# Kernel tuning notes

Measured on AMD Instinct MI355X. Metric: run time of the kernel, lower is better.

The kernel has to match this reference:

```python
import jax, jax.numpy as jnp
import numpy as np

C = 64; H = 80; W = 120; B = 2; V = 3; BV = B * V; D = 20
NEAR = 0.1; FAR = 100.0
BF16 = jnp.bfloat16


def conv2d(x, w, b, pad):
    y = jax.lax.conv_general_dilated(x, w, (1, 1), [(pad, pad), (pad, pad)],
                                     dimension_numbers=('NCHW', 'OIHW', 'NCHW'))
    return y + b[None, :, None, None]


def bn2d(x, g, b, m, v, eps=1e-5):
    # BatchNorm2d in inference mode (running stats)
    scale = g / jnp.sqrt(v + eps)
    return (x - m[None, :, None, None]) * scale[None, :, None, None] + b[None, :, None, None]


def grid_sample(feat, grid):
    # feat [N,C,Hf,Wf], grid [N,Hg,Wg,2] in [-1,1]; bilinear, zeros padding, align_corners=True
    _, _, Hf, Wf = feat.shape
    gx = (grid[..., 0] + 1.0) * 0.5 * (Wf - 1)
    gy = (grid[..., 1] + 1.0) * 0.5 * (Hf - 1)
    x0 = jnp.floor(gx); y0 = jnp.floor(gy)

    def one(f, gx, gy, x0, y0):
        def gather(xi, yi):
            valid = (xi >= 0) & (xi < Wf) & (yi >= 0) & (yi < Hf)
            xc = jnp.clip(xi, 0, Wf - 1).astype(jnp.int32)
            yc = jnp.clip(yi, 0, Hf - 1).astype(jnp.int32)
            return f[:, yc, xc] * valid.astype(f.dtype)
        wx = gx - x0; wy = gy - y0
        return (gather(x0, y0) * ((1 - wx) * (1 - wy))
                + gather(x0 + 1, y0) * (wx * (1 - wy))
                + gather(x0, y0 + 1) * ((1 - wx) * wy)
                + gather(x0 + 1, y0 + 1) * (wx * wy))
    return jax.vmap(one)(feat, gx, gy, x0, y0)


def forward(x, intrinsics, c2ws,
            pf_bn1_g, pf_bn1_b, pf_bn1_m, pf_bn1_v, pf_w1, pf_b1,
            pf_bn2_g, pf_bn2_b, pf_bn2_m, pf_bn2_v, pf_w2, pf_b2,
            cp_w, cp_b, cf_bn_g, cf_bn_b, cf_bn_m, cf_bn_v, cf_w, cf_b):
    # ---- flag[0]: predicted depth -> world xyz, position_fusion ----
    depth = 255.0 * (0.5 * jnp.tanh(x[:, 0]) + 0.5)                       # [BV,H,W]
    d16 = depth.astype(BF16)
    ug = jnp.broadcast_to(jnp.arange(W, dtype=jnp.float32)[None, :], (H, W)).astype(BF16)
    vg = jnp.broadcast_to(jnp.arange(H, dtype=jnp.float32)[:, None], (H, W)).astype(BF16)
    cam = jnp.stack([ug[None] * d16, vg[None] * d16, d16], axis=-1).reshape(BV, H * W, 3)
    Kinv = jnp.linalg.inv(intrinsics.astype(jnp.float32)).astype(BF16)
    xyz = jnp.einsum('nij,npj->npi', Kinv, cam)                           # cam coords
    xyz = jnp.einsum('nij,npj->npi', c2ws[:, :3, :3].astype(BF16), xyz) \
          + c2ws[:, :3, 3].astype(BF16)[:, None, :]                       # world coords
    xyz = xyz.reshape(BV, H, W, 3).transpose(0, 3, 1, 2).astype(x.dtype)
    h = jnp.concatenate([xyz, x], axis=1)                                 # [BV,C+3,H,W]
    h = jax.nn.silu(conv2d(bn2d(h, pf_bn1_g, pf_bn1_b, pf_bn1_m, pf_bn1_v), pf_w1, pf_b1, 4))
    h = jax.nn.silu(conv2d(bn2d(h, pf_bn2_g, pf_bn2_b, pf_bn2_m, pf_bn2_v), pf_w2, pf_b2, 4))

    # ---- flag[1]: multi-view plane-sweep correlation ----
    xr = h.reshape(B, V, C, H, W)
    vb = lambda t: t.transpose(1, 0, 2, 3, 4).reshape(BV, C, H, W)        # 'b v ... -> (v b) ...'
    feat01 = vb(xr)
    Ki = intrinsics.reshape(B, V, 3, 3)
    intr_curr = jax.lax.stop_gradient(
        (Ki * jnp.array([W, H, 1.0], jnp.float32)[None, None, :, None]).transpose(1, 0, 2, 3).reshape(BV, 3, 3))
    E = jax.lax.stop_gradient(c2ws.reshape(B, V, 4, 4))
    Einv = jnp.linalg.inv(E)
    dmin, dmax = 1.0 / FAR, 1.0 / NEAR
    depth_vals = 1.0 / (dmin + jnp.linspace(0.0, 1.0, D) * (dmax - dmin))  # [D]
    pix = jnp.stack([jnp.broadcast_to(jnp.arange(W, dtype=jnp.float32)[None, :], (H, W)),
                     jnp.broadcast_to(jnp.arange(H, dtype=jnp.float32)[:, None], (H, W)),
                     jnp.ones((H, W), jnp.float32)], 0).reshape(3, H * W)
    Kinv_c = jnp.linalg.inv(intr_curr).astype(BF16)

    corr = 0.0
    for idx in range(1, V):
        order = list(range(V))[idx:] + list(range(V))[:idx]
        feat10 = vb(xr[:, jnp.array(order)])                              # [BV,C,H,W]
        pose = jnp.concatenate([E[:, o] @ Einv[:, v0] for v0, o in enumerate(order)], axis=0)  # [BV,4,4]
        pts = jnp.einsum('bij,jp->bip', Kinv_c, pix.astype(BF16))
        pts = jnp.einsum('bij,bjp->bip', pose[:, :3, :3].astype(BF16), pts)
        pts = pts[:, :, None, :] * depth_vals.astype(BF16)[None, None, :, None] \
              + pose[:, :3, 3].astype(BF16)[:, :, None, None]             # [BV,3,D,HW]
        pts = jnp.einsum('bij,bjdp->bidp', intr_curr.astype(BF16), pts).astype(jnp.float32)
        den = jnp.maximum(pts[:, 2], 1e-3)
        grid = jnp.stack([2.0 * pts[:, 0] / den / (W - 1) - 1.0,
                          2.0 * pts[:, 1] / den / (H - 1) - 1.0], axis=-1)
        grid = jax.lax.stop_gradient(grid.reshape(BV, D * H, W, 2))
        warped = grid_sample(feat10, grid).reshape(BV, C, D, H, W)
        corr = corr + jnp.einsum('bchw,bcdhw->bdhw', feat01, warped) / (C ** 0.5)
    corr = corr / (V - 1)

    cin = jnp.concatenate([corr, feat01], axis=1)                         # [BV,D+C,H,W]
    cost = conv2d(cin, cp_w, cp_b, 1).reshape(V, B, C, H, W).transpose(1, 0, 2, 3, 4)
    fused = jnp.concatenate([cost, xr], axis=2).reshape(BV, 2 * C, H, W)
    out = jax.nn.silu(conv2d(bn2d(fused, cf_bn_g, cf_bn_b, cf_bn_m, cf_bn_v), cf_w, cf_b, 4))
    return out


def setup_inputs() -> dict:
    key = jax.random.key(0)
    ks = jax.random.split(key, 24)
    def nrm(i, shape, scale=1.0):
        return scale * jax.random.normal(ks[i], shape, jnp.float32)
    def wconv(i, shape):
        fan_in = int(np.prod(shape[1:]))
        return jax.random.normal(ks[i], shape, jnp.float32) / np.sqrt(fan_in)
    x = nrm(0, (BV, C, H, W))
    Kmat = np.tile(np.array([[1.2, 0, 0.5], [0, 1.6, 0.5], [0, 0, 1.0]], np.float32), (BV, 1, 1))
    intrinsics = jnp.asarray(Kmat)
    c2_list = []
    for i in range(BV):
        th = 0.3 * (i % V) - 0.3
        T = np.eye(4, dtype=np.float32)
        T[:3, :3] = np.array([[np.cos(th), 0, np.sin(th)], [0, 1, 0], [-np.sin(th), 0, np.cos(th)]], np.float32)
        T[:3, 3] = [0.5 * (i % V) - 0.5, 0.0, 0.1]
        c2_list.append(T)
    c2ws = jnp.asarray(np.stack(c2_list))
    # first BN sees raw world-xyz channels (magnitude ~1e4), so realistic running var there
    bn1_v = jnp.concatenate([jnp.full((3,), 1e8, jnp.float32), jnp.ones((C,), jnp.float32)])
    return dict(
        x=x, intrinsics=intrinsics, c2ws=c2ws,
        pf_bn1_g=1.0 + 0.1 * nrm(1, (C + 3,)), pf_bn1_b=0.1 * nrm(2, (C + 3,)),
        pf_bn1_m=0.1 * nrm(3, (C + 3,)), pf_bn1_v=bn1_v,
        pf_w1=wconv(4, (C, C + 3, 9, 9)), pf_b1=0.01 * nrm(5, (C,)),
        pf_bn2_g=1.0 + 0.1 * nrm(6, (C,)), pf_bn2_b=0.1 * nrm(7, (C,)),
        pf_bn2_m=0.1 * nrm(8, (C,)), pf_bn2_v=jnp.ones((C,), jnp.float32),
        pf_w2=wconv(9, (C, C, 9, 9)), pf_b2=0.01 * nrm(10, (C,)),
        cp_w=wconv(11, (C, C + D, 3, 3)), cp_b=0.01 * nrm(12, (C,)),
        cf_bn_g=1.0 + 0.1 * nrm(13, (2 * C,)), cf_bn_b=0.1 * nrm(14, (2 * C,)),
        cf_bn_m=0.1 * nrm(15, (2 * C,)), cf_bn_v=jnp.ones((2 * C,), jnp.float32),
        cf_w=wconv(16, (C, 2 * C, 9, 9)), cf_b=0.01 * nrm(17, (C,)))


def reference(x, intrinsics, c2ws,
              pf_bn1_g, pf_bn1_b, pf_bn1_m, pf_bn1_v, pf_w1, pf_b1,
              pf_bn2_g, pf_bn2_b, pf_bn2_m, pf_bn2_v, pf_w2, pf_b2,
              cp_w, cp_b, cf_bn_g, cf_bn_b, cf_bn_m, cf_bn_v, cf_w, cf_b):
    return forward(x, intrinsics, c2ws,
                   pf_bn1_g, pf_bn1_b, pf_bn1_m, pf_bn1_v, pf_w1, pf_b1,
                   pf_bn2_g, pf_bn2_b, pf_bn2_m, pf_bn2_v, pf_w2, pf_b2,
                   cp_w, cp_b, cf_bn_g, cf_bn_b, cf_bn_m, cf_bn_v, cf_w, cf_b)
```

## Files before the change

kernel.cpp:

```cpp
#include <hip/hip_runtime.h>
#include <math.h>

static constexpr int kH  = 80;
static constexpr int kW  = 120;
static constexpr int kHW = kH * kW;
static constexpr int kBV = 6;
static constexpr int kD  = 20;

typedef __attribute__((ext_vector_type(8)))  short bf16x8;
typedef __attribute__((ext_vector_type(16))) float f32x16;
typedef __attribute__((ext_vector_type(4)))  int   i32x4;
typedef __attribute__((ext_vector_type(2)))  int   i32x2;
typedef __attribute__((ext_vector_type(4)))  float float4v;

__device__ __forceinline__ float bf16r(float x) {
  unsigned u = __float_as_uint(x);
  u += 0x7FFFu + ((u >> 16) & 1u);
  return __uint_as_float(u & 0xFFFF0000u);
}
__device__ __forceinline__ unsigned short bf16c(float x) {
  unsigned u = __float_as_uint(x);
  u += 0x7FFFu + ((u >> 16) & 1u);
  return (unsigned short)(u >> 16);
}
__device__ __forceinline__ int pack2(float a, float b) {
  return (int)((unsigned)bf16c(a) | ((unsigned)bf16c(b) << 16));
}
__device__ __forceinline__ float bl(unsigned pk) {
  return __uint_as_float(pk << 16);
}
__device__ __forceinline__ float bh(unsigned pk) {
  return __uint_as_float(pk & 0xFFFF0000u);
}

struct ConstBuf {
  float bn1_s[67], bn1_o[67];
  float bn2_s[64], bn2_o[64];
  float bnf_s[128], bnf_o[128];
  float Kinv[6][9];
  float Rw[6][9];
  float tw[6][3];
  float Kinvc[6][9];
  float intrc[6][9];
  float poseR[2][6][9];
  float poseT[2][6][3];
  float dvals[20];
};

__device__ void inv3x3(const float* A, float* o) {
  float a = A[0], b = A[1], c = A[2];
  float d = A[3], e = A[4], f = A[5];
  float g = A[6], h = A[7], i = A[8];
  float det = a * (e * i - f * h) - b * (d * i - f * g) + c * (d * h - e * g);
  float id = 1.0f / det;
  o[0] = (e * i - f * h) * id;
  o[1] = -(b * i - c * h) * id;
  o[2] = (b * f - c * e) * id;
  o[3] = -(d * i - f * g) * id;
  o[4] = (a * i - c * g) * id;
  o[5] = -(a * f - c * d) * id;
  o[6] = (d * h - e * g) * id;
  o[7] = -(a * h - b * g) * id;
  o[8] = (a * e - b * d) * id;
}

__device__ void inv4x4(const float* A, float* out) {
  float M[4][8];
  for (int r = 0; r < 4; ++r) {
    for (int c = 0; c < 4; ++c) M[r][c] = A[r * 4 + c];
    for (int c = 0; c < 4; ++c) M[r][4 + c] = (r == c) ? 1.0f : 0.0f;
  }
  for (int col = 0; col < 4; ++col) {
    int p = col;
    float best = fabsf(M[col][col]);
    for (int r = col + 1; r < 4; ++r) {
      float v = fabsf(M[r][col]);
      if (v > best) { best = v; p = r; }
    }
    if (p != col)
      for (int c = 0; c < 8; ++c) { float t = M[col][c]; M[col][c] = M[p][c]; M[p][c] = t; }
    float inv = 1.0f / M[col][col];
    for (int c = 0; c < 8; ++c) M[col][c] *= inv;
    for (int r = 0; r < 4; ++r) {
      if (r == col) continue;
      float f = M[r][col];
      for (int c = 0; c < 8; ++c) M[r][c] -= f * M[col][c];
    }
  }
  for (int r = 0; r < 4; ++r)
    for (int c = 0; c < 4; ++c) out[r * 4 + c] = M[r][4 + c];
}

__device__ void mm4(const float* A, const float* B, float* C) {
  for (int r = 0; r < 4; ++r)
    for (int c = 0; c < 4; ++c) {
      float s = 0.0f;
      for (int k = 0; k < 4; ++k) s += A[r * 4 + k] * B[k * 4 + c];
      C[r * 4 + c] = s;
    }
}

__global__ void consts_kernel(const float* __restrict__ intr, const float* __restrict__ c2,
                              const float* g1, const float* b1, const float* m1, const float* v1,
                              const float* g2, const float* b2, const float* m2, const float* v2,
                              const float* gf, const float* bff, const float* mf, const float* vff,
                              ConstBuf* cb) {
  int tid = threadIdx.x;
  for (int c = tid; c < 67; c += 64) {
    float s = g1[c] / sqrtf(v1[c] + 1e-5f);
    cb->bn1_s[c] = s; cb->bn1_o[c] = b1[c] - m1[c] * s;
  }
  for (int c = tid; c < 64; c += 64) {
    float s = g2[c] / sqrtf(v2[c] + 1e-5f);
    cb->bn2_s[c] = s; cb->bn2_o[c] = b2[c] - m2[c] * s;
  }
  for (int c = tid; c < 128; c += 64) {
    float s = gf[c] / sqrtf(vff[c] + 1e-5f);
    cb->bnf_s[c] = s; cb->bnf_o[c] = bff[c] - mf[c] * s;
  }
  if (tid < 20) {
    float l = (1.0f / 19.0f) * (float)tid;
    cb->dvals[tid] = bf16r(1.0f / (0.01f + l * 9.99f));
  }
  __shared__ float Einv_s[6][16];
  if (tid < 6) {
    float Ki[9];
    inv3x3(intr + tid * 9, Ki);
    for (int k = 0; k < 9; ++k) cb->Kinv[tid][k] = bf16r(Ki[k]);
    const float* T = c2 + tid * 16;
    cb->Rw[tid][0] = bf16r(T[0]);  cb->Rw[tid][1] = bf16r(T[1]);  cb->Rw[tid][2] = bf16r(T[2]);
    cb->Rw[tid][3] = bf16r(T[4]);  cb->Rw[tid][4] = bf16r(T[5]);  cb->Rw[tid][5] = bf16r(T[6]);
    cb->Rw[tid][6] = bf16r(T[8]);  cb->Rw[tid][7] = bf16r(T[9]);  cb->Rw[tid][8] = bf16r(T[10]);
    cb->tw[tid][0] = bf16r(T[3]);  cb->tw[tid][1] = bf16r(T[7]);  cb->tw[tid][2] = bf16r(T[11]);
    inv4x4(T, Einv_s[tid]);
    int vj = tid >> 1, bj = tid & 1, ii = bj * 3 + vj;
    const float* Kk = intr + ii * 9;
    float S[9] = {Kk[0] * 120.0f, Kk[1] * 120.0f, Kk[2] * 120.0f,
                  Kk[3] * 80.0f,  Kk[4] * 80.0f,  Kk[5] * 80.0f,
                  Kk[6],          Kk[7],          Kk[8]};
    for (int k = 0; k < 9; ++k) cb->intrc[tid][k] = bf16r(S[k]);
    float Si[9];
    inv3x3(S, Si);
    for (int k = 0; k < 9; ++k) cb->Kinvc[tid][k] = bf16r(Si[k]);
  }
  __syncthreads();
  if (tid < 12) {
    int t = tid / 6, jj = tid % 6;
    int vj = jj >> 1, bj = jj & 1;
    int o = (vj + t + 1) % 3;
    float P[16];
    mm4(c2 + (bj * 3 + o) * 16, Einv_s[bj * 3 + vj], P);
    for (int r = 0; r < 3; ++r) {
      for (int c = 0; c < 3; ++c) cb->poseR[t][jj][r * 3 + c] = bf16r(P[r * 4 + c]);
      cb->poseT[t][jj][r] = bf16r(P[r * 4 + 3]);
    }
  }
}

template <int K, int CINP, int CINR>
__global__ __launch_bounds__(256)
void prep_w(const float* __restrict__ w, unsigned short* __restrict__ Wp) {
  constexpr int NCH = CINP / 32;
  constexpr int NU = K * K * NCH * 256;
  int u = blockIdx.x * 256 + threadIdx.x;
  if (u >= NU) return;
  int slot = u & 255;
  int rest = u >> 8;
  int ci = rest % NCH;
  int kk = rest / NCH;
  int ky = kk / K, kx = kk - ky * K;
  int oc = slot >> 2;
  int gi = (slot & 3) ^ ((oc >> 2) & 3);
  int chb = ci * 32 + gi * 8;
  unsigned short o[8];
#pragma unroll
  for (int e = 0; e < 8; ++e) {
    int ch = chb + e;
    float val = (ch < CINR) ? w[(((size_t)oc * CINR + ch) * K + ky) * K + kx] : 0.0f;
    o[e] = bf16c(val);
  }
  i32x4 pk;
  pk.x = (int)o[0] | ((int)o[1] << 16);
  pk.y = (int)o[2] | ((int)o[3] << 16);
  pk.z = (int)o[4] | ((int)o[5] << 16);
  pk.w = (int)o[6] | ((int)o[7] << 16);
  *(i32x4*)&Wp[(size_t)u * 8] = pk;
}

__global__ __launch_bounds__(256)
void hn_pack(const float* __restrict__ x, const ConstBuf* __restrict__ cb,
             unsigned short* __restrict__ hn_b) {
  int id = blockIdx.x * 256 + threadIdx.x;
  if (id >= kBV * kHW) return;
  int bv = id / kHW, pix = id - bv * kHW;
  int yy = pix / kW, xx = pix - yy * kW;
  float t0 = tanhf(x[(size_t)bv * 64 * kHW + pix]);
  float depth = 255.0f * (0.5f * t0 + 0.5f);
  float dz = bf16r(depth);
  float cx = bf16r((float)xx * dz);
  float cy = bf16r((float)yy * dz);
  const float* Ki = cb->Kinv[bv];
  float p0 = bf16r(Ki[0] * cx + Ki[1] * cy + Ki[2] * dz);
  float p1 = bf16r(Ki[3] * cx + Ki[4] * cy + Ki[5] * dz);
  float p2 = bf16r(Ki[6] * cx + Ki[7] * cy + Ki[8] * dz);
  const float* R = cb->Rw[bv];
  const float* tw = cb->tw[bv];
  float q[3];
  q[0] = bf16r(bf16r(R[0] * p0 + R[1] * p1 + R[2] * p2) + tw[0]);
  q[1] = bf16r(bf16r(R[3] * p0 + R[4] * p1 + R[5] * p2) + tw[1]);
  q[2] = bf16r(bf16r(R[6] * p0 + R[7] * p1 + R[8] * p2) + tw[2]);
  unsigned short* o = &hn_b[(size_t)id * 96];
  const float* xb = x + (size_t)bv * 64 * kHW + pix;
#pragma unroll
  for (int g = 0; g < 24; ++g) {
    float vv[4];
#pragma unroll
    for (int e = 0; e < 4; ++e) {
      int ch = g * 4 + e;
      float val;
      if (ch < 3) val = q[ch] * cb->bn1_s[ch] + cb->bn1_o[ch];
      else if (ch < 67) val = xb[(size_t)(ch - 3) * kHW] * cb->bn1_s[ch] + cb->bn1_o[ch];
      else val = 0.0f;
      vv[e] = val;
    }
    i32x2 pk = {pack2(vv[0], vv[1]), pack2(vv[2], vv[3])};
    *(i32x2*)(o + g * 4) = pk;
  }
}

template <int CINP, int K, int OUT>
__global__ __launch_bounds__(256)
void conv_mfma(const unsigned short* __restrict__ in_b,
               const unsigned short* __restrict__ Wp,
               const float* __restrict__ bias,
               const ConstBuf* __restrict__ cb,
               float* __restrict__ outf,
               unsigned short* __restrict__ outb,
               unsigned short* __restrict__ outb2) {
  constexpr int NCH = CINP / 32;
  constexpr int KK = K * K;
  constexpr int GN = KK / 3;
  constexpr int PAD = K / 2;
  constexpr int NC = 16 + K - 1;
  constexpr int NR = 8 + K - 1;
  constexpr int NPX = NC * NR;
  __shared__ unsigned short sA[NPX * 32];
  __shared__ unsigned short sB[2][3 * 2048];

  const int tid = threadIdx.x;
  const int w = tid >> 6, l = tid & 63;
  const int bx = blockIdx.x, by = blockIdx.y, bz = blockIdx.z;
  const size_t inbase = (size_t)bz * kHW;

  const int r = l & 31, h = l >> 5;
  const int xloc = r & 15;
  const int ybase = 2 * w + (r >> 4);
  f32x16 acc[2] = {};

  int boff[2][2];
#pragma unroll
  for (int nt = 0; nt < 2; ++nt)
#pragma unroll
    for (int kc = 0; kc < 2; ++kc) {
      int oc = nt * 32 + (l & 31);
      int gi = kc * 2 + h;
      boff[nt][kc] = (oc * 4 + (gi ^ ((oc >> 2) & 3))) * 8;
    }

  for (int ci = 0; ci < NCH; ++ci) {
    for (int g2 = tid; g2 < NPX * 4; g2 += 256) {
      int px = g2 >> 2, gi = g2 & 3;
      int hy = px / NC, hx = px - hy * NC;
      int gy = by * 8 - PAD + hy, gx = bx * 16 - PAD + hx;
      bool ok = ((unsigned)gy < (unsigned)kH) && ((unsigned)gx < (unsigned)kW);
      i32x4 v = {0, 0, 0, 0};
      if (ok) v = *(const i32x4*)&in_b[(inbase + gy * kW + gx) * CINP + ci * 32 + gi * 8];
      *(i32x4*)&sA[px * 32 + ((gi ^ ((px >> 2) & 3)) << 3)] = v;
    }
#pragma unroll
    for (int t = 0; t < 3; ++t) {
      int u = tid + t * 256;
      int kki = u >> 8, slot = u & 255;
      *(i32x4*)&sB[0][u * 8] =
          *(const i32x4*)&Wp[(((size_t)kki * NCH + ci) * 256 + slot) * 8];
    }
    __syncthreads();

    for (int g = 0; g < GN; ++g) {
      const int cur = g & 1, nxt = cur ^ 1;
      const bool hasnext = (g + 1 < GN);
      i32x4 pf[3];
      if (hasnext) {
#pragma unroll
        for (int t = 0; t < 3; ++t) {
          int u = tid + t * 256;
          int kki = u >> 8, slot = u & 255;
          pf[t] = *(const i32x4*)
              &Wp[(((size_t)((g + 1) * 3 + kki) * NCH + ci) * 256 + slot) * 8];
        }
      }
#pragma unroll
      for (int kki = 0; kki < 3; ++kki) {
        const int kk = g * 3 + kki;
        const int ky = kk / K, kx = kk - ky * K;
        const int hp = (ybase + ky) * NC + (xloc + kx);
        bf16x8 a[2];
#pragma unroll
        for (int kc = 0; kc < 2; ++kc) {
          int gi = kc * 2 + h;
          a[kc] = *(const bf16x8*)&sA[hp * 32 + ((gi ^ ((hp >> 2) & 3)) << 3)];
        }
        bf16x8 bb[2][2];
#pragma unroll
        for (int nt = 0; nt < 2; ++nt)
#pragma unroll
          for (int kc = 0; kc < 2; ++kc)
            bb[nt][kc] = *(const bf16x8*)&sB[cur][kki * 2048 + boff[nt][kc]];
#pragma unroll
        for (int nt = 0; nt < 2; ++nt) {
          acc[nt] = __builtin_amdgcn_mfma_f32_32x32x16_bf16(a[0], bb[nt][0], acc[nt], 0, 0, 0);
          acc[nt] = __builtin_amdgcn_mfma_f32_32x32x16_bf16(a[1], bb[nt][1], acc[nt], 0, 0, 0);
        }
      }
      if (hasnext) {
#pragma unroll
        for (int t = 0; t < 3; ++t)
          *(i32x4*)&sB[nxt][(tid + t * 256) * 8] = pf[t];
      }
      __syncthreads();
    }
  }

#pragma unroll
  for (int nt = 0; nt < 2; ++nt) {
    const int oc = nt * 32 + (l & 31);
    const float bs = bias[oc];
    float s2 = 0.f, o2 = 0.f;
    if (OUT == 0) { s2 = cb->bn2_s[oc]; o2 = cb->bn2_o[oc]; }
    if (OUT == 1) { s2 = cb->bnf_s[64 + oc]; o2 = cb->bnf_o[64 + oc]; }
    if (OUT == 2) { s2 = cb->bnf_s[oc]; o2 = cb->bnf_o[oc]; }
#pragma unroll
    for (int reg = 0; reg < 16; ++reg) {
      int row = (reg & 3) + 8 * (reg >> 2) + 4 * h;
      int x = bx * 16 + (row & 15);
      if (x >= kW) continue;
      int y = by * 8 + 2 * w + (row >> 4);
      float v = acc[nt][reg] + bs;
      if (OUT != 2) v = v / (1.0f + expf(-v));
      if (OUT == 0) {
        size_t px = inbase + y * kW + x;
        outb[px * 64 + oc] = bf16c(v * s2 + o2);
      } else if (OUT == 1) {
        size_t px = inbase + y * kW + x;
        outb[px * 64 + oc] = bf16c(v);
        outb2[px * 128 + 64 + oc] = bf16c(v * s2 + o2);
      } else if (OUT == 2) {
        int i = (bz & 1) * 3 + (bz >> 1);
        size_t px = (size_t)i * kHW + y * kW + x;
        outb[px * 128 + oc] = bf16c(v * s2 + o2);
      } else {
        outf[((size_t)bz * 64 + oc) * kHW + y * kW + x] = v;
      }
    }
  }
}

__global__ __launch_bounds__(256)
void corr_kernel(const unsigned short* __restrict__ h_b, const ConstBuf* __restrict__ cb,
                 unsigned short* __restrict__ cin_b) {
  __shared__ float sgeo[4][2][40][8];
  const int tid = threadIdx.x;
  const int w = tid >> 6, lane = tid & 63;
  const int pair = blockIdx.x * 4 + w;
  const int j = pair / (kHW / 2);
  const int pix = (pair - j * (kHW / 2)) * 2;
  const int b = j & 1, v = j >> 1;
  const int ph = lane >> 5, cl = lane & 31;
  const int pixl = pix + ph;
  const int dst = b * 3 + v;
  const unsigned f01pk =
      ((const unsigned*)(h_b + ((size_t)dst * kHW + pixl) * 64))[cl];
  const float f01lo = bl(f01pk), f01hi = bh(f01pk);
  const char* sb0 = (const char*)(h_b + (size_t)(b * 3 + ((v + 1) % 3)) * kHW * 64);
  const char* sb1 = (const char*)(h_b + (size_t)(b * 3 + ((v + 2) % 3)) * kHW * 64);

  for (int job = lane; job < 80; job += 64) {
    const int p = job / 40, jj = job - p * 40;
    const int d = jj >> 1, t = jj & 1;
    const int pp = pix + p;
    const int yyp = pp / kW, xxp = pp - yyp * kW;
    const float* Kc = cb->Kinvc[j];
    const float* IC = cb->intrc[j];
    const float uf = (float)xxp, vf = (float)yyp;
    float p1_0 = bf16r(Kc[0] * uf + Kc[1] * vf + Kc[2]);
    float p1_1 = bf16r(Kc[3] * uf + Kc[4] * vf + Kc[5]);
    float p1_2 = bf16r(Kc[6] * uf + Kc[7] * vf + Kc[8]);
    const float* PR = cb->poseR[t][j];
    const float* PT = cb->poseT[t][j];
    float p20 = bf16r(PR[0] * p1_0 + PR[1] * p1_1 + PR[2] * p1_2);
    float p21 = bf16r(PR[3] * p1_0 + PR[4] * p1_1 + PR[5] * p1_2);
    float p22 = bf16r(PR[6] * p1_0 + PR[7] * p1_1 + PR[8] * p1_2);
    float dv = cb->dvals[d];
    float q0 = bf16r(bf16r(p20 * dv) + PT[0]);
    float q1 = bf16r(bf16r(p21 * dv) + PT[1]);
    float q2 = bf16r(bf16r(p22 * dv) + PT[2]);
    float s0 = bf16r(IC[0] * q0 + IC[1] * q1 + IC[2] * q2);
    float s1 = bf16r(IC[3] * q0 + IC[4] * q1 + IC[5] * q2);
    float s2 = bf16r(IC[6] * q0 + IC[7] * q1 + IC[8] * q2);
    float den = fmaxf(s2, 1e-3f);
    float g0 = 2.0f * s0 / den / 119.0f - 1.0f;
    float g1 = 2.0f * s1 / den / 79.0f - 1.0f;
    float gx = (g0 + 1.0f) * 0.5f * 119.0f;
    float gy = (g1 + 1.0f) * 0.5f * 79.0f;
    float x0f = floorf(gx), y0f = floorf(gy);
    float wx = gx - x0f, wy = gy - y0f;
    float x1f = x0f + 1.0f, y1f = y0f + 1.0f;
    float vx0 = (x0f >= 0.0f && x0f < 120.0f) ? 1.0f : 0.0f;
    float vx1 = (x1f >= 0.0f && x1f < 120.0f) ? 1.0f : 0.0f;
    float vy0 = (y0f >= 0.0f && y0f < 80.0f) ? 1.0f : 0.0f;
    float vy1 = (y1f >= 0.0f && y1f < 80.0f) ? 1.0f : 0.0f;
    int xi0 = (int)fminf(fmaxf(x0f, 0.0f), 119.0f);
    int xi1 = (int)fminf(fmaxf(x1f, 0.0f), 119.0f);
    int yi0 = (int)fminf(fmaxf(y0f, 0.0f), 79.0f);
    int yi1 = (int)fminf(fmaxf(y1f, 0.0f), 79.0f);
    int r0b = yi0 * (kW * 128), r1b = yi1 * (kW * 128);
    int c0b = xi0 * 128, c1b = xi1 * 128;
    float* gp = sgeo[w][p][jj];
    gp[0] = __int_as_float(r0b + c0b);
    gp[1] = __int_as_float(r0b + c1b);
    gp[2] = __int_as_float(r1b + c0b);
    gp[3] = __int_as_float(r1b + c1b);
    gp[4] = ((1.0f - wx) * (1.0f - wy)) * (vx0 * vy0);
    gp[5] = (wx * (1.0f - wy)) * (vx1 * vy0);
    gp[6] = ((1.0f - wx) * wy) * (vx0 * vy1);
    gp[7] = (wx * wy) * (vx1 * vy1);
  }
  __syncthreads();

  unsigned short* op = &cin_b[(size_t)(j * kHW + pixl) * 96];
  *(unsigned*)(op + 20 + 2 * cl) = f01pk;
  if (cl < 6) *(unsigned*)(op + 84 + 2 * cl) = 0u;

  const unsigned cl4 = (unsigned)cl * 4u;
#pragma unroll 2
  for (int d = 0; d < kD; ++d) {
    float a = 0.0f;
#pragma unroll
    for (int t = 0; t < 2; ++t) {
      const char* sb = t ? sb1 : sb0;
      const float* gp = sgeo[w][ph][d * 2 + t];
      float4v ga = *(const float4v*)gp;
      float4v gb = *(const float4v*)(gp + 4);
      unsigned k00 = *(const unsigned*)(sb + ((unsigned)__float_as_int(ga.x) + cl4));
      unsigned k10 = *(const unsigned*)(sb + ((unsigned)__float_as_int(ga.y) + cl4));
      unsigned k01 = *(const unsigned*)(sb + ((unsigned)__float_as_int(ga.z) + cl4));
      unsigned k11 = *(const unsigned*)(sb + ((unsigned)__float_as_int(ga.w) + cl4));
      float al = gb.x * bl(k00) + gb.y * bl(k10) + gb.z * bl(k01) + gb.w * bl(k11);
      float ah = gb.x * bh(k00) + gb.y * bh(k10) + gb.z * bh(k01) + gb.w * bh(k11);
      a += al * f01lo + ah * f01hi;
    }
#pragma unroll
    for (int off = 16; off > 0; off >>= 1) a += __shfl_xor(a, off, 64);
    if (cl == 0) op[d] = bf16c(a * 0.0625f);
  }
}

extern "C" void kernel_launch(void* const* d_in, const int* in_sizes, int n_in,
                              void* d_out, int out_size, void* d_ws, size_t ws_size,
                              hipStream_t stream) {
  (void)in_sizes; (void)n_in; (void)out_size; (void)ws_size;
  const float* x    = (const float*)d_in[0];
  const float* intr = (const float*)d_in[1];
  const float* c2w  = (const float*)d_in[2];
  const float* bn1g = (const float*)d_in[3];
  const float* bn1b = (const float*)d_in[4];
  const float* bn1m = (const float*)d_in[5];
  const float* bn1v = (const float*)d_in[6];
  const float* w1   = (const float*)d_in[7];
  const float* b1   = (const float*)d_in[8];
  const float* bn2g = (const float*)d_in[9];
  const float* bn2b = (const float*)d_in[10];
  const float* bn2m = (const float*)d_in[11];
  const float* bn2v = (const float*)d_in[12];
  const float* w2   = (const float*)d_in[13];
  const float* b2   = (const float*)d_in[14];
  const float* cpw  = (const float*)d_in[15];
  const float* cpb  = (const float*)d_in[16];
  const float* bnfg = (const float*)d_in[17];
  const float* bnfb = (const float*)d_in[18];
  const float* bnfm = (const float*)d_in[19];
  const float* bnfv = (const float*)d_in[20];
  const float* wf   = (const float*)d_in[21];
  const float* bff  = (const float*)d_in[22];

  char* ws = (char*)d_ws;
  ConstBuf* cb            = (ConstBuf*)ws;
  unsigned short* hn_b    = (unsigned short*)(ws + 8192);
  unsigned short* h1_b    = (unsigned short*)(ws + 11067392);
  unsigned short* h_b     = (unsigned short*)(ws + 18440192);
  unsigned short* cin_b   = (unsigned short*)(ws + 33185792);
  unsigned short* fused_b = (unsigned short*)(ws + 44244992);
  unsigned short* Wp1     = (unsigned short*)(ws + 58990592);
  unsigned short* Wp2     = (unsigned short*)(ws + 59985920);
  unsigned short* Wpc     = (unsigned short*)(ws + 60649472);
  unsigned short* Wpf     = (unsigned short*)(ws + 60760064);

  consts_kernel<<<1, 64, 0, stream>>>(intr, c2w, bn1g, bn1b, bn1m, bn1v,
                                      bn2g, bn2b, bn2m, bn2v, bnfg, bnfb, bnfm, bnfv, cb);
  prep_w<9, 96, 67><<<243, 256, 0, stream>>>(w1, Wp1);
  prep_w<9, 64, 64><<<162, 256, 0, stream>>>(w2, Wp2);
  prep_w<3, 96, 84><<<27, 256, 0, stream>>>(cpw, Wpc);
  prep_w<9, 128, 128><<<324, 256, 0, stream>>>(wf, Wpf);
  hn_pack<<<225, 256, 0, stream>>>(x, cb, hn_b);

  dim3 cgrid(8, 10, 6);
  conv_mfma<96, 9, 0><<<cgrid, 256, 0, stream>>>(hn_b, Wp1, b1, cb, nullptr, h1_b, nullptr);
  conv_mfma<64, 9, 1><<<cgrid, 256, 0, stream>>>(h1_b, Wp2, b2, cb, nullptr, h_b, fused_b);
  corr_kernel<<<7200, 256, 0, stream>>>(h_b, cb, cin_b);
  conv_mfma<96, 3, 2><<<cgrid, 256, 0, stream>>>(cin_b, Wpc, cpb, cb, nullptr, fused_b, nullptr);
  conv_mfma<128, 9, 3><<<cgrid, 256, 0, stream>>>(fused_b, Wpf, bff, cb, (float*)d_out, nullptr, nullptr);
}
```

Before: 340.6 us.

## Split conv kernel-tap loop across wave pairs and load weights directly to registers

Restructures the MFMA convolution so each wave computes a 2x2 tile of 32x32 blocks (two pixel row-pairs by two output-channel halves). The kernel taps are split between two wave halves, whose partial sums are reduced through shared memory at the end. Weights are repacked so each lane reads its B fragments straight from global memory into registers, double-buffered. This removes the shared-memory weight staging and the per-tap-group barriers, and increases A/B reuse per wave. The cost is more accumulator registers, an LDS reduction step, and uncoalesced-but-cached weight reads from global memory.

```diff
diff --git a/kernel.cpp b/kernel.cpp
--- a/kernel.cpp
+++ b/kernel.cpp
@@ -169,8 +169,10 @@
   int ci = rest % NCH;
   int kk = rest / NCH;
   int ky = kk / K, kx = kk - ky * K;
-  int oc = slot >> 2;
-  int gi = (slot & 3) ^ ((oc >> 2) & 3);
+  int q = slot >> 6, lu = slot & 63;
+  int nt = q >> 1, kc = q & 1;
+  int oc = nt * 32 + (lu & 31);
+  int gi = kc * 2 + (lu >> 5);
   int chb = ci * 32 + gi * 8;
   unsigned short o[8];
 #pragma unroll
@@ -239,35 +241,27 @@
                unsigned short* __restrict__ outb2) {
   constexpr int NCH = CINP / 32;
   constexpr int KK = K * K;
-  constexpr int GN = KK / 3;
+  constexpr int KH0 = (KK + 1) / 2;
   constexpr int PAD = K / 2;
   constexpr int NC = 16 + K - 1;
   constexpr int NR = 8 + K - 1;
   constexpr int NPX = NC * NR;
   __shared__ unsigned short sA[NPX * 32];
-  __shared__ unsigned short sB[2][3 * 2048];
 
   const int tid = threadIdx.x;
   const int w = tid >> 6, l = tid & 63;
+  const int half = w >> 1, mp = w & 1;
   const int bx = blockIdx.x, by = blockIdx.y, bz = blockIdx.z;
   const size_t inbase = (size_t)bz * kHW;
 
   const int r = l & 31, h = l >> 5;
-  const int xloc = r & 15;
-  const int ybase = 2 * w + (r >> 4);
-  f32x16 acc[2] = {};
-
-  int boff[2][2];
-#pragma unroll
-  for (int nt = 0; nt < 2; ++nt)
-#pragma unroll
-    for (int kc = 0; kc < 2; ++kc) {
-      int oc = nt * 32 + (l & 31);
-      int gi = kc * 2 + h;
-      boff[nt][kc] = (oc * 4 + (gi ^ ((oc >> 2) & 3))) * 8;
-    }
+  const int xloc = r & 15, rhi = r >> 4;
+  const int kk0 = half ? KH0 : 0;
+  const int myKK = half ? (KK - KH0) : KH0;
+  f32x16 acc[2][2] = {};
 
   for (int ci = 0; ci < NCH; ++ci) {
+    __syncthreads();
     for (int g2 = tid; g2 < NPX * 4; g2 += 256) {
       int px = g2 >> 2, gi = g2 & 3;
       int hy = px / NC, hx = px - hy * NC;
@@ -277,89 +271,107 @@
       if (ok) v = *(const i32x4*)&in_b[(inbase + gy * kW + gx) * CINP + ci * 32 + gi * 8];
       *(i32x4*)&sA[px * 32 + ((gi ^ ((px >> 2) & 3)) << 3)] = v;
     }
-#pragma unroll
-    for (int t = 0; t < 3; ++t) {
-      int u = tid + t * 256;
-      int kki = u >> 8, slot = u & 255;
-      *(i32x4*)&sB[0][u * 8] =
-          *(const i32x4*)&Wp[(((size_t)kki * NCH + ci) * 256 + slot) * 8];
-    }
     __syncthreads();
 
-    for (int g = 0; g < GN; ++g) {
-      const int cur = g & 1, nxt = cur ^ 1;
-      const bool hasnext = (g + 1 < GN);
-      i32x4 pf[3];
-      if (hasnext) {
-#pragma unroll
-        for (int t = 0; t < 3; ++t) {
-          int u = tid + t * 256;
-          int kki = u >> 8, slot = u & 255;
-          pf[t] = *(const i32x4*)
-              &Wp[(((size_t)((g + 1) * 3 + kki) * NCH + ci) * 256 + slot) * 8];
-        }
-      }
-#pragma unroll
-      for (int kki = 0; kki < 3; ++kki) {
-        const int kk = g * 3 + kki;
-        const int ky = kk / K, kx = kk - ky * K;
-        const int hp = (ybase + ky) * NC + (xloc + kx);
-        bf16x8 a[2];
-#pragma unroll
-        for (int kc = 0; kc < 2; ++kc) {
-          int gi = kc * 2 + h;
-          a[kc] = *(const bf16x8*)&sA[hp * 32 + ((gi ^ ((hp >> 2) & 3)) << 3)];
-        }
-        bf16x8 bb[2][2];
-#pragma unroll
-        for (int nt = 0; nt < 2; ++nt)
-#pragma unroll
-          for (int kc = 0; kc < 2; ++kc)
-            bb[nt][kc] = *(const bf16x8*)&sB[cur][kki * 2048 + boff[nt][kc]];
-#pragma unroll
-        for (int nt = 0; nt < 2; ++nt) {
-          acc[nt] = __builtin_amdgcn_mfma_f32_32x32x16_bf16(a[0], bb[nt][0], acc[nt], 0, 0, 0);
-          acc[nt] = __builtin_amdgcn_mfma_f32_32x32x16_bf16(a[1], bb[nt][1], acc[nt], 0, 0, 0);
-        }
-      }
-      if (hasnext) {
-#pragma unroll
-        for (int t = 0; t < 3; ++t)
-          *(i32x4*)&sB[nxt][(tid + t * 256) * 8] = pf[t];
+    const unsigned short* wb = Wp + ((size_t)ci * 256 + (size_t)kk0 * NCH * 256) * 8;
+    const size_t kstep = (size_t)NCH * 256 * 8;
+#define LOADB(dst, rdidx)                                                       \
+    {                                                                           \
+      const unsigned short* bp = wb + (size_t)(rdidx) * kstep + (size_t)l * 8;  \
+      dst[0][0] = *(const bf16x8*)(bp);                                         \
+      dst[0][1] = *(const bf16x8*)(bp + 64 * 8);                                \
+      dst[1][0] = *(const bf16x8*)(bp + 128 * 8);                               \
+      dst[1][1] = *(const bf16x8*)(bp + 192 * 8);                               \
+    }
+#define COMPUTE(rdidx, bb)                                                      \
+    {                                                                           \
+      const int kk = kk0 + (rdidx);                                             \
+      const int ky = kk / K, kx = kk - ky * K;                                  \
+      bf16x8 a[2][2];                                                           \
+      _Pragma("unroll")                                                         \
+      for (int m = 0; m < 2; ++m) {                                             \
+        const int hp = (4 * mp + 2 * m + rhi + ky) * NC + (xloc + kx);          \
+        _Pragma("unroll")                                                       \
+        for (int kc = 0; kc < 2; ++kc) {                                        \
+          int gi = kc * 2 + h;                                                  \
+          a[m][kc] = *(const bf16x8*)&sA[hp * 32 + ((gi ^ ((hp >> 2) & 3)) << 3)]; \
+        }                                                                       \
+      }                                                                         \
+      _Pragma("unroll")                                                         \
+      for (int m = 0; m < 2; ++m)                                               \
+        _Pragma("unroll")                                                       \
+        for (int nt = 0; nt < 2; ++nt) {                                        \
+          acc[m][nt] = __builtin_amdgcn_mfma_f32_32x32x16_bf16(a[m][0], bb[nt][0], acc[m][nt], 0, 0, 0); \
+          acc[m][nt] = __builtin_amdgcn_mfma_f32_32x32x16_bf16(a[m][1], bb[nt][1], acc[m][nt], 0, 0, 0); \
+        }                                                                       \
+    }
+
+    bf16x8 b0[2][2], b1[2][2];
+    LOADB(b0, 0);
+    int rd = 0;
+    for (; rd + 2 <= myKK; rd += 2) {
+      LOADB(b1, rd + 1);
+      COMPUTE(rd, b0);
+      if (rd + 2 < myKK) LOADB(b0, rd + 2);
+      COMPUTE(rd + 1, b1);
+    }
+    if (rd < myKK) COMPUTE(rd, b0);
+#undef LOADB
+#undef COMPUTE
+  }
+
+  float* scratch = (float*)sA;
+#pragma unroll
+  for (int cm = 0; cm < 2; ++cm) {
+#pragma unroll
+    for (int cn = 0; cn < 2; ++cn) {
+      float* sp = scratch + ((mp * 64 + l) * 16);
+      __syncthreads();
+      if (half == 1) {
+#pragma unroll
+        for (int q = 0; q < 16; ++q) sp[q] = acc[cm][cn][q];
       }
       __syncthreads();
-    }
-  }
-
-#pragma unroll
-  for (int nt = 0; nt < 2; ++nt) {
-    const int oc = nt * 32 + (l & 31);
-    const float bs = bias[oc];
-    float s2 = 0.f, o2 = 0.f;
-    if (OUT == 0) { s2 = cb->bn2_s[oc]; o2 = cb->bn2_o[oc]; }
-    if (OUT == 1) { s2 = cb->bnf_s[64 + oc]; o2 = cb->bnf_o[64 + oc]; }
-    if (OUT == 2) { s2 = cb->bnf_s[oc]; o2 = cb->bnf_o[oc]; }
-#pragma unroll
-    for (int reg = 0; reg < 16; ++reg) {
-      int row = (reg & 3) + 8 * (reg >> 2) + 4 * h;
-      int x = bx * 16 + (row & 15);
-      if (x >= kW) continue;
-      int y = by * 8 + 2 * w + (row >> 4);
-      float v = acc[nt][reg] + bs;
-      if (OUT != 2) v = v / (1.0f + expf(-v));
-      if (OUT == 0) {
-        size_t px = inbase + y * kW + x;
-        outb[px * 64 + oc] = bf16c(v * s2 + o2);
-      } else if (OUT == 1) {
-        size_t px = inbase + y * kW + x;
-        outb[px * 64 + oc] = bf16c(v);
-        outb2[px * 128 + 64 + oc] = bf16c(v * s2 + o2);
-      } else if (OUT == 2) {
-        int i = (bz & 1) * 3 + (bz >> 1);
-        size_t px = (size_t)i * kHW + y * kW + x;
-        outb[px * 128 + oc] = bf16c(v * s2 + o2);
-      } else {
-        outf[((size_t)bz * 64 + oc) * kHW + y * kW + x] = v;
+      if (half == 0) {
+#pragma unroll
+        for (int q = 0; q < 16; ++q) acc[cm][cn][q] += sp[q];
+      }
+    }
+  }
+  if (half == 1) return;
+
+#pragma unroll
+  for (int m = 0; m < 2; ++m) {
+#pragma unroll
+    for (int nt = 0; nt < 2; ++nt) {
+      const int oc = nt * 32 + (l & 31);
+      const float bs = bias[oc];
+      float s2 = 0.f, o2 = 0.f;
+      if (OUT == 0) { s2 = cb->bn2_s[oc]; o2 = cb->bn2_o[oc]; }
+      if (OUT == 1) { s2 = cb->bnf_s[64 + oc]; o2 = cb->bnf_o[64 + oc]; }
+      if (OUT == 2) { s2 = cb->bnf_s[oc]; o2 = cb->bnf_o[oc]; }
+#pragma unroll
+      for (int reg = 0; reg < 16; ++reg) {
+        int row = (reg & 3) + 8 * (reg >> 2) + 4 * h;
+        int x = bx * 16 + (row & 15);
+        if (x >= kW) continue;
+        int y = by * 8 + 4 * mp + 2 * m + (row >> 4);
+        float v = acc[m][nt][reg] + bs;
+        if (OUT != 2) v = v / (1.0f + expf(-v));
+        if (OUT == 0) {
+          size_t px = inbase + y * kW + x;
+          outb[px * 64 + oc] = bf16c(v * s2 + o2);
+        } else if (OUT == 1) {
+          size_t px = inbase + y * kW + x;
+          outb[px * 64 + oc] = bf16c(v);
+          outb2[px * 128 + 64 + oc] = bf16c(v * s2 + o2);
+        } else if (OUT == 2) {
+          int i = (bz & 1) * 3 + (bz >> 1);
+          size_t px = (size_t)i * kHW + y * kW + x;
+          outb[px * 128 + oc] = bf16c(v * s2 + o2);
+        } else {
+          outf[((size_t)bz * 64 + oc) * kHW + y * kW + x] = v;
+        }
       }
     }
   }
```

New measurement: 339.3 us. No clear change (-0.4%).
